# Kernel tuning notes

Measured on AMD Instinct MI355X. Metric: run time of the kernel, lower is better.

The kernel has to match this reference:

```python
import jax, jax.numpy as jnp
import numpy as np

LOG_STD_MAX = 2.0
LOG_STD_MIN = -5.0
LN_EPS = 1e-5


def layer_norm(x, scale, bias):
    mu = jnp.mean(x, axis=-1, keepdims=True)
    var = jnp.var(x, axis=-1, keepdims=True)
    return (x - mu) * jax.lax.rsqrt(var + LN_EPS) * scale + bias


def setup_inputs() -> dict:
    key = jax.random.key(0)
    B, OBS, ACT, H, M, K = 4096, 256, 32, 512, 16, 4
    ks = jax.random.split(key, 8)
    def w(k, shape, fan_in):
        return (jax.random.normal(k, shape, jnp.float32) / np.sqrt(fan_in)).astype(jnp.float32)
    return {
        "x": jax.random.normal(ks[0], (B, OBS), jnp.float32),
        "gate_W": w(ks[1], (OBS, M), OBS),
        "gate_b": jnp.zeros((M,), jnp.float32),
        "fc1_W": w(ks[2], (OBS, H * M), OBS),
        "fc1_b": jnp.zeros((H * M,), jnp.float32),
        "norm1_scale": jnp.ones((H * M,), jnp.float32),
        "norm1_bias": jnp.zeros((H * M,), jnp.float32),
        "fc2_W": w(ks[3], (H * M, H * M), H * M),
        "fc2_b": jnp.zeros((H * M,), jnp.float32),
        "norm2_scale": jnp.ones((H * M,), jnp.float32),
        "norm2_bias": jnp.zeros((H * M,), jnp.float32),
        "mean_W": w(ks[4], (H, ACT), H),
        "mean_b": jnp.zeros((ACT,), jnp.float32),
        "logstd_W": w(ks[5], (H, ACT), H),
        "logstd_b": jnp.zeros((ACT,), jnp.float32),
        "topk": K,
    }


def reference(x, gate_W, gate_b, fc1_W, fc1_b, norm1_scale, norm1_bias,
              fc2_W, fc2_b, norm2_scale, norm2_bias,
              mean_W, mean_b, logstd_W, logstd_b, topk):
    B = x.shape[0]
    M = gate_W.shape[1]
    # gating: softmax -> topk -> renormalize -> scatter into full [B, M] scores
    gate_scores = jax.nn.softmax(x @ gate_W + gate_b, axis=-1)  # [B, M]
    topk_vals, topk_idx = jax.lax.top_k(gate_scores, topk)       # [B, K]
    topk_vals = topk_vals / jnp.sum(topk_vals, axis=-1, keepdims=True)
    scores = jnp.zeros_like(gate_scores).at[jnp.arange(B)[:, None], topk_idx].set(topk_vals)
    # trunk: Linear -> LayerNorm -> ReLU, twice
    h = jax.nn.relu(layer_norm(x @ fc1_W + fc1_b, norm1_scale, norm1_bias))
    h = jax.nn.relu(layer_norm(h @ fc2_W + fc2_b, norm2_scale, norm2_bias))
    # reshape [B, H*M] -> [B, H, M] (expert m = strided slice), weighted MEAN over experts
    h = h.reshape(B, -1, M)                                      # [B, H, M]
    mixed = jnp.einsum('bhm,bm->bh', h, scores) / M              # mean, not sum
    mean = mixed @ mean_W + mean_b
    log_std = jnp.tanh(mixed @ logstd_W + logstd_b)
    log_std = LOG_STD_MIN + 0.5 * (LOG_STD_MAX - LOG_STD_MIN) * (log_std + 1.0)
    return mean, log_std
```

## Files before the change

### kernel.cpp

```cpp
#include <hip/hip_runtime.h>
#include <hip/hip_bf16.h>

typedef unsigned int u32;
typedef unsigned short u16;
typedef __bf16 bf16x8 __attribute__((ext_vector_type(8)));
typedef float f32x4 __attribute__((ext_vector_type(4)));

__device__ __forceinline__ u16 f2b(float f) {
    __bf16 b = (__bf16)f;
    return __builtin_bit_cast(u16, b);
}
__device__ __forceinline__ float b2f(u16 v) {
    u32 x = ((u32)v) << 16;
    return __builtin_bit_cast(float, x);
}

__device__ __forceinline__ void gld_lds16(const void* g, void* l) {
    __builtin_amdgcn_global_load_lds(
        (const __attribute__((address_space(1))) u32*)(size_t)g,
        (__attribute__((address_space(3))) u32*)(u32)(size_t)l,
        16, 0, 0);
}

#define BARRIER __builtin_amdgcn_s_barrier()
#define LGKM0 asm volatile("s_waitcnt lgkmcnt(0)" ::: "memory")
#define VMC4 asm volatile("s_waitcnt vmcnt(4)" ::: "memory")
#define VMC6 asm volatile("s_waitcnt vmcnt(6)" ::: "memory")
#define VMC0 asm volatile("s_waitcnt vmcnt(0)" ::: "memory")
#define MFMA16(d, a, b) d = __builtin_amdgcn_mfma_f32_16x16x32_bf16(a, b, d, 0, 0, 0)

__global__ __launch_bounds__(256) void castgate_kernel(
    const float* __restrict__ x, const float* __restrict__ gW,
    const float* __restrict__ gb, const int* __restrict__ topk,
    u16* __restrict__ XB, float* __restrict__ scores)
{
    const int t = threadIdx.x;
    {
        int i = blockIdx.x * 256 + t;
        float4 f = reinterpret_cast<const float4*>(x)[i];
        u32 lo = (u32)f2b(f.x) | ((u32)f2b(f.y) << 16);
        u32 hi = (u32)f2b(f.z) | ((u32)f2b(f.w) << 16);
        uint2 o; o.x = lo; o.y = hi;
        reinterpret_cast<uint2*>(XB)[i] = o;
    }
    const int row = blockIdx.x * 4 + (t >> 6);
    const int l = t & 63;
    const int m = l & 15;
    const int q = l >> 4;
    const int Kk = *topk;
    const float* xr = x + (long)row * 256;
    float p = 0.f;
    #pragma unroll
    for (int k4 = 0; k4 < 16; ++k4) {
        f32x4 xv = *reinterpret_cast<const f32x4*>(xr + q * 64 + k4 * 4);
        const int kb = q * 64 + k4 * 4;
        p += xv[0] * gW[(kb + 0) * 16 + m] + xv[1] * gW[(kb + 1) * 16 + m]
           + xv[2] * gW[(kb + 2) * 16 + m] + xv[3] * gW[(kb + 3) * 16 + m];
    }
    p += __shfl_xor(p, 16);
    p += __shfl_xor(p, 32);
    float logit = p + gb[m];
    float mx = logit;
    #pragma unroll
    for (int d = 1; d < 16; d <<= 1) mx = fmaxf(mx, __shfl_xor(mx, d));
    int rank = 0;
    #pragma unroll
    for (int j = 0; j < 16; ++j) {
        float vj = __shfl(logit, (l & 48) | j);
        rank += (vj > logit) || (vj == logit && j < m);
    }
    bool sel = rank < Kk;
    float e = sel ? expf(logit - mx) : 0.f;
    float ssum = e;
    #pragma unroll
    for (int d = 1; d < 16; d <<= 1) ssum += __shfl_xor(ssum, d);
    if (q == 0) scores[row * 16 + m] = e / ssum;
}

__global__ __launch_bounds__(256) void transpose_both_kernel(
    const float* __restrict__ w2, u16* __restrict__ W2T,
    const float* __restrict__ w1, u16* __restrict__ W1T)
{
    __shared__ float tile[64][65];
    const int t = threadIdx.x;
    const int byy = blockIdx.y;
    const float* in;
    u16* outp;
    int R, r0;
    if (byy < 128) { in = w2; outp = W2T; R = 8192; r0 = byy * 64; }
    else           { in = w1; outp = W1T; R = 256;  r0 = (byy - 128) * 64; }
    const int C = 8192;
    const int c0 = blockIdx.x * 64;
    #pragma unroll
    for (int i = 0; i < 4; ++i) {
        int idx = t + i * 256;
        int r = idx >> 4;
        int c = (idx & 15) * 4;
        float4 f = *reinterpret_cast<const float4*>(&in[(long)(r0 + r) * C + c0 + c]);
        tile[r][c] = f.x; tile[r][c + 1] = f.y; tile[r][c + 2] = f.z; tile[r][c + 3] = f.w;
    }
    __syncthreads();
    #pragma unroll
    for (int i = 0; i < 4; ++i) {
        int idx = t + i * 256;
        int rr = idx >> 4;
        int cc = idx & 15;
        u32 p0 = (u32)f2b(tile[cc * 4 + 0][rr]) | ((u32)f2b(tile[cc * 4 + 1][rr]) << 16);
        u32 p1 = (u32)f2b(tile[cc * 4 + 2][rr]) | ((u32)f2b(tile[cc * 4 + 3][rr]) << 16);
        uint2 o2; o2.x = p0; o2.y = p1;
        *reinterpret_cast<uint2*>(&outp[(long)(c0 + rr) * R + r0 + cc * 4]) = o2;
    }
}


template<int GRAN>
__device__ __forceinline__ void stage_half(
    const u16* __restrict__ src, int ld, int rowbase, int kk,
    u16* ldsregion, int h, int w, int l)
{
    #pragma unroll
    for (int j = 0; j < 2; ++j) {
        const int c = w * 2 + j;
        const int o = c * 1024 + l * 16;
        const int os = o ^ (((o >> 7) & 7) << 4);
        const int pos = o >> 7;
        const int row = ((pos / GRAN) * 2 + h) * GRAN + (pos & (GRAN - 1));
        const u16* g = src + (long)(rowbase + row) * ld + kk + ((os & 127) >> 1);
        gld_lds16(g, ldsregion + c * 512);
    }
}

__device__ __forceinline__ bf16x8 ldfrag(const u16* region, int pos, int col) {
    const int o = (pos * 128 + col * 2) ^ ((pos & 7) << 4);
    return *reinterpret_cast<const bf16x8*>(reinterpret_cast<const char*>(region) + o);
}

template<int CB>
__device__ __forceinline__ void ktile_group(
    const u16* __restrict__ A, int lda, const u16* __restrict__ BT, int ldb,
    int brow, int bcol, int kkA1, int kkR,
    int wr, int wc, int r4, int q8, int w, int l,
    u16 (&lds)[2][4][8192], f32x4 (&acc)[8][4],
    bf16x8 (&bLu)[2][2], bf16x8 (&bLf)[2][2])
{
    bf16x8 aL[4][2], aH[4][2], bH[2][2];

    #pragma unroll
    for (int m = 0; m < 4; ++m) {
        aL[m][0] = ldfrag(lds[CB][0], wr * 64 + m * 16 + r4, q8);
        aL[m][1] = ldfrag(lds[CB][0], wr * 64 + m * 16 + r4, 32 + q8);
    }
    stage_half<64>(A, lda, brow, kkA1, &lds[1 - CB][1][0], 1, w, l);
    BARRIER; LGKM0;
    __builtin_amdgcn_s_setprio(1);
    #pragma unroll
    for (int m = 0; m < 4; ++m)
        #pragma unroll
        for (int n = 0; n < 2; ++n) {
            MFMA16(acc[m][n], aL[m][0], bLu[n][0]);
            MFMA16(acc[m][n], aL[m][1], bLu[n][1]);
        }
    __builtin_amdgcn_s_setprio(0);
    BARRIER;

    #pragma unroll
    for (int n = 0; n < 2; ++n) {
        bH[n][0] = ldfrag(lds[CB][3], wc * 32 + n * 16 + r4, q8);
        bH[n][1] = ldfrag(lds[CB][3], wc * 32 + n * 16 + r4, 32 + q8);
    }
    stage_half<64>(A, lda, brow, kkR, &lds[CB][0][0], 0, w, l);
    BARRIER; LGKM0;
    __builtin_amdgcn_s_setprio(1);
    #pragma unroll
    for (int m = 0; m < 4; ++m)
        #pragma unroll
        for (int n = 0; n < 2; ++n) {
            MFMA16(acc[m][2 + n], aL[m][0], bH[n][0]);
            MFMA16(acc[m][2 + n], aL[m][1], bH[n][1]);
        }
    __builtin_amdgcn_s_setprio(0);
    BARRIER;

    #pragma unroll
    for (int m = 0; m < 4; ++m) {
        aH[m][0] = ldfrag(lds[CB][1], wr * 64 + m * 16 + r4, q8);
        aH[m][1] = ldfrag(lds[CB][1], wr * 64 + m * 16 + r4, 32 + q8);
    }
    stage_half<32>(BT, ldb, bcol, kkR, &lds[CB][2][0], 0, w, l);
    BARRIER; LGKM0;
    __builtin_amdgcn_s_setprio(1);
    #pragma unroll
    for (int m = 0; m < 4; ++m)
        #pragma unroll
        for (int n = 0; n < 2; ++n) {
            MFMA16(acc[4 + m][2 + n], aH[m][0], bH[n][0]);
            MFMA16(acc[4 + m][2 + n], aH[m][1], bH[n][1]);
        }
    __builtin_amdgcn_s_setprio(0);
    VMC4;
    BARRIER;

    stage_half<32>(BT, ldb, bcol, kkR, &lds[CB][3][0], 1, w, l);
    #pragma unroll
    for (int n = 0; n < 2; ++n) {
        bLf[n][0] = ldfrag(lds[1 - CB][2], wc * 32 + n * 16 + r4, q8);
        bLf[n][1] = ldfrag(lds[1 - CB][2], wc * 32 + n * 16 + r4, 32 + q8);
    }
    __builtin_amdgcn_s_setprio(1);
    #pragma unroll
    for (int m = 0; m < 4; ++m)
        #pragma unroll
        for (int n = 0; n < 2; ++n) {
            MFMA16(acc[4 + m][n], aH[m][0], bLu[n][0]);
            MFMA16(acc[4 + m][n], aH[m][1], bLu[n][1]);
        }
    __builtin_amdgcn_s_setprio(0);
    BARRIER;
}

__global__ __launch_bounds__(512, 2) void gemm256(
    const u16* __restrict__ A, int lda,
    const u16* __restrict__ BT, int ldb,
    u16* __restrict__ C, int ldc, int K)
{
    __shared__ __align__(16) u16 lds[2][4][8192];
    const int t = threadIdx.x;
    const int w = t >> 6, l = t & 63;
    const int wr = w >> 2, wc = w & 3;
    const int r4 = l & 15, q8 = (l >> 4) * 8;
    const int bid = blockIdx.y * 32 + blockIdx.x;
    const int xcd = bid & 7, within = bid >> 3;
    const int by = (xcd >> 2) * 8 + (within >> 3);
    const int bx = (xcd & 3) * 8 + (within & 7);
    const int brow = by * 256, bcol = bx * 256;
    const int NT = K >> 6;

    f32x4 acc[8][4];
    #pragma unroll
    for (int m = 0; m < 8; ++m)
        #pragma unroll
        for (int n = 0; n < 4; ++n)
            acc[m][n] = (f32x4){0.f, 0.f, 0.f, 0.f};

    stage_half<64>(A, lda, brow, 0, &lds[0][0][0], 0, w, l);
    stage_half<32>(BT, ldb, bcol, 0, &lds[0][2][0], 0, w, l);
    stage_half<32>(BT, ldb, bcol, 0, &lds[0][3][0], 1, w, l);
    stage_half<64>(A, lda, brow, 0, &lds[0][1][0], 1, w, l);
    stage_half<64>(A, lda, brow, 64, &lds[1][0][0], 0, w, l);
    stage_half<32>(BT, ldb, bcol, 64, &lds[1][2][0], 0, w, l);
    stage_half<32>(BT, ldb, bcol, 64, &lds[1][3][0], 1, w, l);
    VMC6;
    BARRIER;

    bf16x8 bl0[2][2], bl1[2][2];
    #pragma unroll
    for (int n = 0; n < 2; ++n) {
        bl0[n][0] = ldfrag(lds[0][2], wc * 32 + n * 16 + r4, q8);
        bl0[n][1] = ldfrag(lds[0][2], wc * 32 + n * 16 + r4, 32 + q8);
    }

    for (int i = 0; i < (NT >> 1); ++i) {
        const int U = 2 * i;
        int tV = U + 1;
        int tU2 = U + 2;
        int tV2 = U + 3;
        if (tU2 >= NT) tU2 -= NT;
        if (tV2 >= NT) tV2 -= NT;
        const int kkV = (tV >= NT ? tV - NT : tV) << 6;
        const int kkU2 = tU2 << 6;
        const int kkV2 = tV2 << 6;

        ktile_group<0>(A, lda, BT, ldb, brow, bcol, kkV, kkU2,
                       wr, wc, r4, q8, w, l, lds, acc, bl0, bl1);
        ktile_group<1>(A, lda, BT, ldb, brow, bcol, kkU2, kkV2,
                       wr, wc, r4, q8, w, l, lds, acc, bl1, bl0);
    }

    VMC0;

    const int crow0 = (l >> 4) * 4;
    const int ccol = l & 15;
    #pragma unroll
    for (int m = 0; m < 8; ++m) {
        #pragma unroll
        for (int n = 0; n < 4; ++n) {
            int gr = brow + wr * 128 + m * 16 + crow0;
            int gc = bcol + wc * 64 + n * 16 + ccol;
            #pragma unroll
            for (int r = 0; r < 4; ++r)
                C[(long)(gr + r) * ldc + gc] = f2b(acc[m][n][r]);
        }
    }
}

__global__ __launch_bounds__(256) void ln1_kernel(
    const u16* __restrict__ Y, const float* __restrict__ fcb,
    const float* __restrict__ g, const float* __restrict__ be,
    u16* __restrict__ H)
{
    const int N = 8192;
    const int row = blockIdx.x;
    const int t = threadIdx.x;
    const u16* y = Y + (long)row * N;
    const int base = t * 32;
    float v[32];
    float s = 0.f, s2 = 0.f;
    #pragma unroll
    for (int j = 0; j < 4; ++j) {
        uint4 q = *reinterpret_cast<const uint4*>(y + base + j * 8);
        f32x4 cA = *reinterpret_cast<const f32x4*>(fcb + base + j * 8);
        f32x4 cB = *reinterpret_cast<const f32x4*>(fcb + base + j * 8 + 4);
        const u32 ww[4] = {q.x, q.y, q.z, q.w};
        const float cb[8] = {cA[0], cA[1], cA[2], cA[3], cB[0], cB[1], cB[2], cB[3]};
        #pragma unroll
        for (int e = 0; e < 4; ++e) {
            float a0 = b2f((u16)(ww[e] & 0xffff)) + cb[e * 2];
            float a1 = b2f((u16)(ww[e] >> 16)) + cb[e * 2 + 1];
            v[j * 8 + e * 2] = a0; v[j * 8 + e * 2 + 1] = a1;
            s += a0 + a1;
            s2 += a0 * a0 + a1 * a1;
        }
    }
    #pragma unroll
    for (int d = 32; d > 0; d >>= 1) { s += __shfl_down(s, d); s2 += __shfl_down(s2, d); }
    __shared__ float red[8];
    if ((t & 63) == 0) { red[t >> 6] = s; red[4 + (t >> 6)] = s2; }
    __syncthreads();
    s = red[0] + red[1] + red[2] + red[3];
    s2 = red[4] + red[5] + red[6] + red[7];
    float mu = s * (1.f / N);
    float var = s2 * (1.f / N) - mu * mu;
    float rs = rsqrtf(var + 1e-5f);
    __align__(16) u16 o[32];
    #pragma unroll
    for (int j = 0; j < 4; ++j) {
        f32x4 gA = *reinterpret_cast<const f32x4*>(g + base + j * 8);
        f32x4 gB = *reinterpret_cast<const f32x4*>(g + base + j * 8 + 4);
        f32x4 eA = *reinterpret_cast<const f32x4*>(be + base + j * 8);
        f32x4 eB = *reinterpret_cast<const f32x4*>(be + base + j * 8 + 4);
        const float gg[8] = {gA[0], gA[1], gA[2], gA[3], gB[0], gB[1], gB[2], gB[3]};
        const float ee[8] = {eA[0], eA[1], eA[2], eA[3], eB[0], eB[1], eB[2], eB[3]};
        #pragma unroll
        for (int k = 0; k < 8; ++k) {
            float z = (v[j * 8 + k] - mu) * rs * gg[k] + ee[k];
            o[j * 8 + k] = f2b(fmaxf(z, 0.f));
        }
    }
    u16* h = H + (long)row * N + base;
    #pragma unroll
    for (int j = 0; j < 4; ++j)
        *reinterpret_cast<uint4*>(h + j * 8) = *reinterpret_cast<const uint4*>(&o[j * 8]);
}

__global__ __launch_bounds__(256) void ln2_mix_heads_kernel(
    const u16* __restrict__ Y, const float* __restrict__ fcb,
    const float* __restrict__ g, const float* __restrict__ be,
    const float* __restrict__ scores,
    const float* __restrict__ mW, const float* __restrict__ mb,
    const float* __restrict__ sW, const float* __restrict__ sb,
    float* __restrict__ out)
{
    const int N = 8192;
    const int B = 4096;
    const int row = blockIdx.x;
    const int t = threadIdx.x;
    const u16* y = Y + (long)row * N;
    const int base = t * 32;
    __shared__ float sc[16];
    if (t < 16) sc[t] = scores[row * 16 + t];
    float v[32];
    float s = 0.f, s2 = 0.f;
    #pragma unroll
    for (int j = 0; j < 4; ++j) {
        uint4 q = *reinterpret_cast<const uint4*>(y + base + j * 8);
        f32x4 cA = *reinterpret_cast<const f32x4*>(fcb + base + j * 8);
        f32x4 cB = *reinterpret_cast<const f32x4*>(fcb + base + j * 8 + 4);
        const u32 ww[4] = {q.x, q.y, q.z, q.w};
        const float cb[8] = {cA[0], cA[1], cA[2], cA[3], cB[0], cB[1], cB[2], cB[3]};
        #pragma unroll
        for (int e = 0; e < 4; ++e) {
            float a0 = b2f((u16)(ww[e] & 0xffff)) + cb[e * 2];
            float a1 = b2f((u16)(ww[e] >> 16)) + cb[e * 2 + 1];
            v[j * 8 + e * 2] = a0; v[j * 8 + e * 2 + 1] = a1;
            s += a0 + a1;
            s2 += a0 * a0 + a1 * a1;
        }
    }
    #pragma unroll
    for (int d = 32; d > 0; d >>= 1) { s += __shfl_down(s, d); s2 += __shfl_down(s2, d); }
    __shared__ float red[8];
    if ((t & 63) == 0) { red[t >> 6] = s; red[4 + (t >> 6)] = s2; }
    __syncthreads();
    s = red[0] + red[1] + red[2] + red[3];
    s2 = red[4] + red[5] + red[6] + red[7];
    float mu = s * (1.f / N);
    float var = s2 * (1.f / N) - mu * mu;
    float rs = rsqrtf(var + 1e-5f);
    float m0 = 0.f, m1 = 0.f;
    #pragma unroll
    for (int j = 0; j < 4; ++j) {
        f32x4 g0 = *reinterpret_cast<const f32x4*>(g + base + j * 4);
        f32x4 e0 = *reinterpret_cast<const f32x4*>(be + base + j * 4);
        f32x4 g1 = *reinterpret_cast<const f32x4*>(g + base + 16 + j * 4);
        f32x4 e1 = *reinterpret_cast<const f32x4*>(be + base + 16 + j * 4);
        #pragma unroll
        for (int k = 0; k < 4; ++k) {
            int m = j * 4 + k;
            float z0 = fmaxf((v[m] - mu) * rs * g0[k] + e0[k], 0.f);
            float z1 = fmaxf((v[16 + m] - mu) * rs * g1[k] + e1[k], 0.f);
            m0 += z0 * sc[m];
            m1 += z1 * sc[m];
        }
    }
    __shared__ float mix[512];
    mix[2 * t]     = m0 * (1.f / 16.f);
    mix[2 * t + 1] = m1 * (1.f / 16.f);
    __syncthreads();
    const int a = t & 31;
    const int seg = t >> 5;
    float pm = 0.f, ps = 0.f;
    #pragma unroll 4
    for (int h = seg * 64; h < seg * 64 + 64; ++h) {
        float xv = mix[h];
        pm += xv * mW[h * 32 + a];
        ps += xv * sW[h * 32 + a];
    }
    __shared__ float prm[8][32];
    __shared__ float prs[8][32];
    prm[seg][a] = pm;
    prs[seg][a] = ps;
    __syncthreads();
    if (t < 32) {
        float am = mb[t];
        #pragma unroll
        for (int ss = 0; ss < 8; ++ss) am += prm[ss][t];
        out[(long)row * 32 + t] = am;
    } else if (t < 64) {
        int aa = t - 32;
        float as = sb[aa];
        #pragma unroll
        for (int ss = 0; ss < 8; ++ss) as += prs[ss][aa];
        float ts = tanhf(as);
        out[(long)B * 32 + (long)row * 32 + aa] = -5.0f + 3.5f * (ts + 1.0f);
    }
}

extern "C" void kernel_launch(void* const* d_in, const int* in_sizes, int n_in,
                              void* d_out, int out_size, void* d_ws, size_t ws_size,
                              hipStream_t stream) {
    const float* x   = (const float*)d_in[0];
    const float* gW  = (const float*)d_in[1];
    const float* gb  = (const float*)d_in[2];
    const float* w1  = (const float*)d_in[3];
    const float* b1  = (const float*)d_in[4];
    const float* g1  = (const float*)d_in[5];
    const float* be1 = (const float*)d_in[6];
    const float* w2  = (const float*)d_in[7];
    const float* b2  = (const float*)d_in[8];
    const float* g2  = (const float*)d_in[9];
    const float* be2 = (const float*)d_in[10];
    const float* mW  = (const float*)d_in[11];
    const float* mb  = (const float*)d_in[12];
    const float* sW  = (const float*)d_in[13];
    const float* sb  = (const float*)d_in[14];
    const int* topk  = (const int*)d_in[15];
    float* out = (float*)d_out;

    char* ws = (char*)d_ws;
    u16* W2T = (u16*)ws;            ws += (long)8192 * 8192 * 2;
    u16* Yb = (u16*)ws;             ws += (long)4096 * 8192 * 2;
    u16* H1 = (u16*)ws;             ws += (long)4096 * 8192 * 2;
    u16* W1T = (u16*)ws;            ws += (long)8192 * 256 * 2;
    u16* XB = (u16*)ws;             ws += (long)4096 * 256 * 2;
    float* SCR = (float*)ws;        ws += (long)4096 * 16 * 4;

    castgate_kernel<<<1024, 256, 0, stream>>>(x, gW, gb, topk, XB, SCR);
    transpose_both_kernel<<<dim3(128, 132), 256, 0, stream>>>(w2, W2T, w1, W1T);

    gemm256<<<dim3(32, 16), 512, 0, stream>>>(XB, 256, W1T, 256, Yb, 8192, 256);
    ln1_kernel<<<4096, 256, 0, stream>>>(Yb, b1, g1, be1, H1);

    gemm256<<<dim3(32, 16), 512, 0, stream>>>(H1, 8192, W2T, 8192, Yb, 8192, 8192);
    ln2_mix_heads_kernel<<<4096, 256, 0, stream>>>(Yb, b2, g2, be2, SCR,
                                                   mW, mb, sW, sb, out);
}
```

Measured before the change: 704.6 us.

## Fuse weight transposes into cast-gate and fc1 GEMM launches to overlap work

The W1 transpose moves into the cast/gate kernel as extra blocks, and the large W2 transpose/cast to bf16 moves into the fc1 GEMM launch as extra blocks. Those blocks use the GEMM's shared memory as a 128x64 tile and write 16-byte vectors. This removes a separate launch and lets the memory-bound transpose overlap the small fc1 GEMM. In exchange, the transpose blocks run with 512-thread, 2-per-CU occupancy limits and a larger LDS allocation, which may slow them down.

```diff
diff --git a/kernel.cpp b/kernel.cpp
--- a/kernel.cpp
+++ b/kernel.cpp
@@ -28,89 +28,6 @@
 #define VMC6 asm volatile("s_waitcnt vmcnt(6)" ::: "memory")
 #define VMC0 asm volatile("s_waitcnt vmcnt(0)" ::: "memory")
 #define MFMA16(d, a, b) d = __builtin_amdgcn_mfma_f32_16x16x32_bf16(a, b, d, 0, 0, 0)
-
-__global__ __launch_bounds__(256) void castgate_kernel(
-    const float* __restrict__ x, const float* __restrict__ gW,
-    const float* __restrict__ gb, const int* __restrict__ topk,
-    u16* __restrict__ XB, float* __restrict__ scores)
-{
-    const int t = threadIdx.x;
-    {
-        int i = blockIdx.x * 256 + t;
-        float4 f = reinterpret_cast<const float4*>(x)[i];
-        u32 lo = (u32)f2b(f.x) | ((u32)f2b(f.y) << 16);
-        u32 hi = (u32)f2b(f.z) | ((u32)f2b(f.w) << 16);
-        uint2 o; o.x = lo; o.y = hi;
-        reinterpret_cast<uint2*>(XB)[i] = o;
-    }
-    const int row = blockIdx.x * 4 + (t >> 6);
-    const int l = t & 63;
-    const int m = l & 15;
-    const int q = l >> 4;
-    const int Kk = *topk;
-    const float* xr = x + (long)row * 256;
-    float p = 0.f;
-    #pragma unroll
-    for (int k4 = 0; k4 < 16; ++k4) {
-        f32x4 xv = *reinterpret_cast<const f32x4*>(xr + q * 64 + k4 * 4);
-        const int kb = q * 64 + k4 * 4;
-        p += xv[0] * gW[(kb + 0) * 16 + m] + xv[1] * gW[(kb + 1) * 16 + m]
-           + xv[2] * gW[(kb + 2) * 16 + m] + xv[3] * gW[(kb + 3) * 16 + m];
-    }
-    p += __shfl_xor(p, 16);
-    p += __shfl_xor(p, 32);
-    float logit = p + gb[m];
-    float mx = logit;
-    #pragma unroll
-    for (int d = 1; d < 16; d <<= 1) mx = fmaxf(mx, __shfl_xor(mx, d));
-    int rank = 0;
-    #pragma unroll
-    for (int j = 0; j < 16; ++j) {
-        float vj = __shfl(logit, (l & 48) | j);
-        rank += (vj > logit) || (vj == logit && j < m);
-    }
-    bool sel = rank < Kk;
-    float e = sel ? expf(logit - mx) : 0.f;
-    float ssum = e;
-    #pragma unroll
-    for (int d = 1; d < 16; d <<= 1) ssum += __shfl_xor(ssum, d);
-    if (q == 0) scores[row * 16 + m] = e / ssum;
-}
-
-__global__ __launch_bounds__(256) void transpose_both_kernel(
-    const float* __restrict__ w2, u16* __restrict__ W2T,
-    const float* __restrict__ w1, u16* __restrict__ W1T)
-{
-    __shared__ float tile[64][65];
-    const int t = threadIdx.x;
-    const int byy = blockIdx.y;
-    const float* in;
-    u16* outp;
-    int R, r0;
-    if (byy < 128) { in = w2; outp = W2T; R = 8192; r0 = byy * 64; }
-    else           { in = w1; outp = W1T; R = 256;  r0 = (byy - 128) * 64; }
-    const int C = 8192;
-    const int c0 = blockIdx.x * 64;
-    #pragma unroll
-    for (int i = 0; i < 4; ++i) {
-        int idx = t + i * 256;
-        int r = idx >> 4;
-        int c = (idx & 15) * 4;
-        float4 f = *reinterpret_cast<const float4*>(&in[(long)(r0 + r) * C + c0 + c]);
-        tile[r][c] = f.x; tile[r][c + 1] = f.y; tile[r][c + 2] = f.z; tile[r][c + 3] = f.w;
-    }
-    __syncthreads();
-    #pragma unroll
-    for (int i = 0; i < 4; ++i) {
-        int idx = t + i * 256;
-        int rr = idx >> 4;
-        int cc = idx & 15;
-        u32 p0 = (u32)f2b(tile[cc * 4 + 0][rr]) | ((u32)f2b(tile[cc * 4 + 1][rr]) << 16);
-        u32 p1 = (u32)f2b(tile[cc * 4 + 2][rr]) | ((u32)f2b(tile[cc * 4 + 3][rr]) << 16);
-        uint2 o2; o2.x = p0; o2.y = p1;
-        *reinterpret_cast<uint2*>(&outp[(long)(c0 + rr) * R + r0 + cc * 4]) = o2;
-    }
-}
 
 
 template<int GRAN>
@@ -218,17 +135,16 @@
     BARRIER;
 }
 
-__global__ __launch_bounds__(512, 2) void gemm256(
+__device__ __forceinline__ void gemm_body(
+    int bid, int t,
     const u16* __restrict__ A, int lda,
     const u16* __restrict__ BT, int ldb,
-    u16* __restrict__ C, int ldc, int K)
-{
-    __shared__ __align__(16) u16 lds[2][4][8192];
-    const int t = threadIdx.x;
+    u16* __restrict__ C, int ldc, int K,
+    u16 (&lds)[2][4][8192])
+{
     const int w = t >> 6, l = t & 63;
     const int wr = w >> 2, wc = w & 3;
     const int r4 = l & 15, q8 = (l >> 4) * 8;
-    const int bid = blockIdx.y * 32 + blockIdx.x;
     const int xcd = bid & 7, within = bid >> 3;
     const int by = (xcd >> 2) * 8 + (within >> 3);
     const int bx = (xcd & 3) * 8 + (within & 7);
@@ -291,6 +207,130 @@
                 C[(long)(gr + r) * ldc + gc] = f2b(acc[m][n][r]);
         }
     }
+}
+
+__global__ __launch_bounds__(512, 2) void gemm256(
+    const u16* __restrict__ A, int lda,
+    const u16* __restrict__ BT, int ldb,
+    u16* __restrict__ C, int ldc, int K)
+{
+    __shared__ __align__(16) u16 lds[2][4][8192];
+    gemm_body(blockIdx.y * 32 + blockIdx.x, threadIdx.x,
+              A, lda, BT, ldb, C, ldc, K, lds);
+}
+
+__global__ __launch_bounds__(512, 2) void fc1_w2t_kernel(
+    const u16* __restrict__ XB, const u16* __restrict__ W1T,
+    u16* __restrict__ Yb,
+    const float* __restrict__ w2, u16* __restrict__ W2T)
+{
+    __shared__ __align__(16) u16 lds[2][4][8192];
+    const int t = threadIdx.x;
+    if (blockIdx.x < 512) {
+        gemm_body(blockIdx.x, t, XB, 256, W1T, 256, Yb, 8192, 256, lds);
+        return;
+    }
+    float (*tile)[65] = reinterpret_cast<float(*)[65]>(&lds[0][0][0]);
+    const int tid = blockIdx.x - 512;
+    const int ct = tid & 127, rt = tid >> 7;
+    const int r0 = rt * 128, c0 = ct * 64;
+    #pragma unroll
+    for (int i = 0; i < 4; ++i) {
+        int idx = t + i * 512;
+        int r = idx >> 4;
+        int c = (idx & 15) * 4;
+        float4 f = *reinterpret_cast<const float4*>(&w2[(long)(r0 + r) * 8192 + c0 + c]);
+        tile[r][c] = f.x; tile[r][c + 1] = f.y; tile[r][c + 2] = f.z; tile[r][c + 3] = f.w;
+    }
+    __syncthreads();
+    const int rr = t >> 3;
+    const int ch = t & 7;
+    u32 pk[8];
+    #pragma unroll
+    for (int j = 0; j < 8; ++j) {
+        int cc = ch * 16 + j * 2;
+        pk[j] = (u32)f2b(tile[cc][rr]) | ((u32)f2b(tile[cc + 1][rr]) << 16);
+    }
+    u16* dst = &W2T[(long)(c0 + rr) * 8192 + r0 + ch * 16];
+    uint4 o0; o0.x = pk[0]; o0.y = pk[1]; o0.z = pk[2]; o0.w = pk[3];
+    uint4 o1; o1.x = pk[4]; o1.y = pk[5]; o1.z = pk[6]; o1.w = pk[7];
+    reinterpret_cast<uint4*>(dst)[0] = o0;
+    reinterpret_cast<uint4*>(dst)[1] = o1;
+}
+
+__global__ __launch_bounds__(256) void castgate_w1t_kernel(
+    const float* __restrict__ x, const float* __restrict__ gW,
+    const float* __restrict__ gb, const int* __restrict__ topk,
+    u16* __restrict__ XB, float* __restrict__ scores,
+    const float* __restrict__ w1, u16* __restrict__ W1T)
+{
+    const int t = threadIdx.x;
+    if (blockIdx.x >= 1024) {
+        __shared__ float tile[64][65];
+        const int tid = blockIdx.x - 1024;
+        const int ct = tid & 127, rt = tid >> 7;
+        const int r0 = rt * 64, c0 = ct * 64;
+        #pragma unroll
+        for (int i = 0; i < 4; ++i) {
+            int idx = t + i * 256;
+            int r = idx >> 4;
+            int c = (idx & 15) * 4;
+            float4 f = *reinterpret_cast<const float4*>(&w1[(long)(r0 + r) * 8192 + c0 + c]);
+            tile[r][c] = f.x; tile[r][c + 1] = f.y; tile[r][c + 2] = f.z; tile[r][c + 3] = f.w;
+        }
+        __syncthreads();
+        #pragma unroll
+        for (int i = 0; i < 4; ++i) {
+            int idx = t + i * 256;
+            int rr = idx >> 4;
+            int cc = idx & 15;
+            u32 p0 = (u32)f2b(tile[cc * 4 + 0][rr]) | ((u32)f2b(tile[cc * 4 + 1][rr]) << 16);
+            u32 p1 = (u32)f2b(tile[cc * 4 + 2][rr]) | ((u32)f2b(tile[cc * 4 + 3][rr]) << 16);
+            uint2 o2; o2.x = p0; o2.y = p1;
+            *reinterpret_cast<uint2*>(&W1T[(long)(c0 + rr) * 256 + r0 + cc * 4]) = o2;
+        }
+        return;
+    }
+    {
+        int i = blockIdx.x * 256 + t;
+        float4 f = reinterpret_cast<const float4*>(x)[i];
+        u32 lo = (u32)f2b(f.x) | ((u32)f2b(f.y) << 16);
+        u32 hi = (u32)f2b(f.z) | ((u32)f2b(f.w) << 16);
+        uint2 o; o.x = lo; o.y = hi;
+        reinterpret_cast<uint2*>(XB)[i] = o;
+    }
+    const int row = blockIdx.x * 4 + (t >> 6);
+    const int l = t & 63;
+    const int m = l & 15;
+    const int q = l >> 4;
+    const int Kk = *topk;
+    const float* xr = x + (long)row * 256;
+    float p = 0.f;
+    #pragma unroll
+    for (int k4 = 0; k4 < 16; ++k4) {
+        f32x4 xv = *reinterpret_cast<const f32x4*>(xr + q * 64 + k4 * 4);
+        const int kb = q * 64 + k4 * 4;
+        p += xv[0] * gW[(kb + 0) * 16 + m] + xv[1] * gW[(kb + 1) * 16 + m]
+           + xv[2] * gW[(kb + 2) * 16 + m] + xv[3] * gW[(kb + 3) * 16 + m];
+    }
+    p += __shfl_xor(p, 16);
+    p += __shfl_xor(p, 32);
+    float logit = p + gb[m];
+    float mx = logit;
+    #pragma unroll
+    for (int d = 1; d < 16; d <<= 1) mx = fmaxf(mx, __shfl_xor(mx, d));
+    int rank = 0;
+    #pragma unroll
+    for (int j = 0; j < 16; ++j) {
+        float vj = __shfl(logit, (l & 48) | j);
+        rank += (vj > logit) || (vj == logit && j < m);
+    }
+    bool sel = rank < Kk;
+    float e = sel ? expf(logit - mx) : 0.f;
+    float ssum = e;
+    #pragma unroll
+    for (int d = 1; d < 16; d <<= 1) ssum += __shfl_xor(ssum, d);
+    if (q == 0) scores[row * 16 + m] = e / ssum;
 }
 
 __global__ __launch_bounds__(256) void ln1_kernel(
@@ -474,13 +514,14 @@
     u16* XB = (u16*)ws;             ws += (long)4096 * 256 * 2;
     float* SCR = (float*)ws;        ws += (long)4096 * 16 * 4;
 
-    castgate_kernel<<<1024, 256, 0, stream>>>(x, gW, gb, topk, XB, SCR);
-    transpose_both_kernel<<<dim3(128, 132), 256, 0, stream>>>(w2, W2T, w1, W1T);
-
-    gemm256<<<dim3(32, 16), 512, 0, stream>>>(XB, 256, W1T, 256, Yb, 8192, 256);
+    castgate_w1t_kernel<<<1536, 256, 0, stream>>>(x, gW, gb, topk, XB, SCR, w1, W1T);
+
+    fc1_w2t_kernel<<<512 + 8192, 512, 0, stream>>>(XB, W1T, Yb, w2, W2T);
+
     ln1_kernel<<<4096, 256, 0, stream>>>(Yb, b1, g1, be1, H1);
 
     gemm256<<<dim3(32, 16), 512, 0, stream>>>(H1, 8192, W2T, 8192, Yb, 8192, 8192);
+
     ln2_mix_heads_kernel<<<4096, 256, 0, stream>>>(Yb, b2, g2, be2, SCR,
                                                    mW, mb, sW, sb, out);
 }
```

Result: slower. 728.4 us (+3.4%).
